# Kernel optimization log

Hardware: AMD Instinct MI355X
Metric: run time of the kernel (lower is better)

Reference implementation:

```python
import jax, jax.numpy as jnp
import numpy as np

ALPHA = 0.9
EPS = 0.01
LAMBDA_PENALTY = 1.0
THRESHOLD = 0.8
COS_EPS = 1e-8
N, F, E = 8192, 256, 262144


def setup_inputs() -> dict:
    key = jax.random.key(0)
    k1, k2, k3, k4, k5 = jax.random.split(key, 5)
    z = jax.random.normal(k1, (N, F), dtype=jnp.float32)
    x_hat = jax.random.normal(k2, (N, F), dtype=jnp.float32)
    edge_index = jax.random.randint(k3, (2, E), 0, N, dtype=jnp.int64)
    f_k2u = jax.random.randint(k4, (N,), 0, 6, dtype=jnp.int64)
    f_u2k = jax.random.randint(k5, (N,), 0, 32, dtype=jnp.int64)
    return {"z": z, "x_hat": x_hat, "edge_index": edge_index,
            "f_k2u": f_k2u, "f_u2k": f_u2k, "epoch": 10}


def _corrcoef_features(z):
    # torch.corrcoef(z.T): correlation between the F feature columns over N nodes
    zm = z - jnp.mean(z, axis=0, keepdims=True)        # [N, F]
    cov = zm.T @ zm                                    # [F, F] (scale cancels in corr)
    std = jnp.sqrt(jnp.diag(cov))                      # [F]
    cor = cov / (std[:, None] * std[None, :])
    cor = jnp.clip(jnp.nan_to_num(cor), -1.0, 1.0)
    # fill_diagonal_(0)
    return cor * (1.0 - jnp.eye(cor.shape[0], dtype=cor.dtype))


def reference(z, x_hat, edge_index, f_k2u, f_u2k, epoch):
    n, f = z.shape
    zm = z - jnp.mean(z, axis=0, keepdims=True)
    cor = _corrcoef_features(z)                        # [F, F]
    # per-node scalar weight: alpha**f_k2u + (1 - alpha**f_u2k)
    w = (ALPHA ** f_k2u.astype(z.dtype)
         + (1.0 - ALPHA ** f_u2k.astype(z.dtype)))     # [N]
    W = w[:, None] * zm                                # [N, F]
    z2 = z + EPS * (W @ cor)                           # [N, F]

    # homophily (crash=True): per-edge cosine sim, scatter-add by source, degree-normalize
    i, j = edge_index[0], edge_index[1]
    zi, zj = z2[i], z2[j]                              # [E, F] gathers
    num = jnp.sum(zi * zj, axis=1)
    ni = jnp.maximum(jnp.linalg.norm(zi, axis=1), COS_EPS)
    nj = jnp.maximum(jnp.linalg.norm(zj, axis=1), COS_EPS)
    sim = num / (ni * nj)                              # [E]
    scores = jax.ops.segment_sum(sim, i, num_segments=n)
    deg = jax.ops.segment_sum(jnp.ones_like(sim), i, num_segments=n)
    deg = jnp.where(deg == 0, 1.0, deg)
    homophily_loss = -jnp.mean(scores / deg)

    # extra_loss (crash=True): dense NxN similarity masked by dense adjacency
    sim_mat = z2 @ z2.T                                # [N, N]
    adj = jnp.zeros((n, n), dtype=z.dtype)
    adj = adj.at[i, j].set(1.0).at[j, i].set(1.0)
    non_conn = sim_mat * (1.0 - adj)
    penalty = jnp.mean(jnp.where(non_conn > THRESHOLD, non_conn, 0.0))

    return homophily_loss + LAMBDA_PENALTY * penalty
```

## Files before the change

kernel.cpp:

```cpp
#include <hip/hip_runtime.h>
#include <stdint.h>
#include <math.h>

#define EPS_C 0.01f
#define THRESH 0.8f

constexpr int Nn = 8192;
constexpr int Ff = 256;
constexpr int Ee = 262144;

__device__ __forceinline__ float b2f(unsigned short u) {
  union { uint32_t i; float f; } v; v.i = ((uint32_t)u) << 16; return v.f;
}
__device__ __forceinline__ unsigned short f2b(float f) {
  union { uint32_t i; float f; } v; v.f = f;
  uint32_t r = v.i + 0x7FFFu + ((v.i >> 16) & 1u);
  return (unsigned short)(r >> 16);
}

typedef __bf16 bf16x8 __attribute__((ext_vector_type(8)));
typedef float f32x4 __attribute__((ext_vector_type(4)));

__global__ void k_transpose(const float* __restrict__ z, unsigned short* __restrict__ zT,
                            float* __restrict__ colsum) {
  __shared__ float Ls[64][65];
  int n0 = blockIdx.x * 64;
  int c0 = blockIdx.y * 64;
  int t = threadIdx.x;
  int r = t >> 4;
  int cq = t & 15;
#pragma unroll
  for (int i = 0; i < 4; ++i) {
    int row = r + 16 * i;
    float4 v = *(const float4*)(z + (size_t)(n0 + row) * Ff + c0 + cq * 4);
    Ls[row][cq * 4 + 0] = v.x;
    Ls[row][cq * 4 + 1] = v.y;
    Ls[row][cq * 4 + 2] = v.z;
    Ls[row][cq * 4 + 3] = v.w;
  }
  __syncthreads();
  if (t < 64) {
    float s = 0.f;
#pragma unroll
    for (int rr = 0; rr < 64; ++rr) s += Ls[rr][t];
    atomicAdd(&colsum[c0 + t], s);
  }
  int cr = t >> 4;
  int nq = t & 15;
#pragma unroll
  for (int i = 0; i < 4; ++i) {
    int c = cr + 16 * i;
    ushort4 o;
    o.x = f2b(Ls[nq * 4 + 0][c]);
    o.y = f2b(Ls[nq * 4 + 1][c]);
    o.z = f2b(Ls[nq * 4 + 2][c]);
    o.w = f2b(Ls[nq * 4 + 3][c]);
    *(ushort4*)(zT + (size_t)(c0 + c) * Nn + n0 + nq * 4) = o;
  }
}

__global__ __launch_bounds__(256, 2) void k_covg(const unsigned short* __restrict__ zT,
                                                 float* __restrict__ covp) {
  int bx = blockIdx.x, by = blockIdx.y, p = blockIdx.z;
  __shared__ __align__(16) unsigned short As[128 * 64];
  __shared__ __align__(16) unsigned short Bs[128 * 64];
  int t = threadIdx.x;
  int lane = t & 63, wv = t >> 6;
  int wr = wv >> 1, wc = wv & 1;
  int quad = lane >> 4, l15 = lane & 15;
  int a0 = by * 128, b0 = bx * 128;

  f32x4 acc[4][4];
#pragma unroll
  for (int i = 0; i < 4; ++i)
#pragma unroll
    for (int j = 0; j < 4; ++j) acc[i][j] = (f32x4){0.f, 0.f, 0.f, 0.f};

  for (int kk = 0; kk < 8; ++kk) {
    int k0 = p * 512 + kk * 64;
#pragma unroll
    for (int it = 0; it < 4; ++it) {
      int s = it * 256 + t;
      int r = s >> 3;
      int g = (s & 7) ^ (r & 7);
      const unsigned short* ga = zT + (size_t)(a0 + r) * Nn + k0 + g * 8;
      const unsigned short* gb = zT + (size_t)(b0 + r) * Nn + k0 + g * 8;
      __builtin_amdgcn_global_load_lds((const __attribute__((address_space(1))) void*)ga,
                                       (__attribute__((address_space(3))) void*)(As + s * 8),
                                       16, 0, 0);
      __builtin_amdgcn_global_load_lds((const __attribute__((address_space(1))) void*)gb,
                                       (__attribute__((address_space(3))) void*)(Bs + s * 8),
                                       16, 0, 0);
    }
    __syncthreads();
#pragma unroll
    for (int kc = 0; kc < 2; ++kc) {
      bf16x8 afr[4], bfr[4];
#pragma unroll
      for (int mt = 0; mt < 4; ++mt) {
        int rA = wr * 64 + mt * 16 + l15;
        int g = kc * 4 + quad;
        int gl = g ^ (rA & 7);
        afr[mt] = *(const bf16x8*)(As + ((size_t)rA * 8 + gl) * 8);
      }
#pragma unroll
      for (int nt = 0; nt < 4; ++nt) {
        int rB = wc * 64 + nt * 16 + l15;
        int g = kc * 4 + quad;
        int gl = g ^ (rB & 7);
        bfr[nt] = *(const bf16x8*)(Bs + ((size_t)rB * 8 + gl) * 8);
      }
#pragma unroll
      for (int mt = 0; mt < 4; ++mt)
#pragma unroll
        for (int nt = 0; nt < 4; ++nt)
          acc[mt][nt] = __builtin_amdgcn_mfma_f32_16x16x32_bf16(afr[mt], bfr[nt],
                                                                acc[mt][nt], 0, 0, 0);
    }
    __syncthreads();
  }

  float* outp = covp + (size_t)p * 65536;
#pragma unroll
  for (int mt = 0; mt < 4; ++mt)
#pragma unroll
    for (int r = 0; r < 4; ++r) {
      int a = a0 + wr * 64 + mt * 16 + quad * 4 + r;
#pragma unroll
      for (int nt = 0; nt < 4; ++nt) {
        int b = b0 + wc * 64 + nt * 16 + l15;
        outp[(size_t)a * Ff + b] = acc[mt][nt][r];
      }
    }
}

__global__ void k_cor(const float* __restrict__ covp, const float* __restrict__ colsum,
                      float* __restrict__ cor) {
  __shared__ float sd[256];
  int a = blockIdx.x, b = threadIdx.x;
  float mb = colsum[b] * (1.f / 8192.f);
  float gb = 0.f;
#pragma unroll
  for (int p = 0; p < 16; ++p) gb += covp[(size_t)p * 65536 + b * 257];
  float sb = sqrtf(gb - 8192.f * mb * mb);
  sd[b] = sb;
  float g = 0.f;
#pragma unroll
  for (int p = 0; p < 16; ++p) g += covp[(size_t)p * 65536 + a * Ff + b];
  __syncthreads();
  float c = 0.f;
  if (a != b) {
    float ma = colsum[a] * (1.f / 8192.f);
    float cv = g - 8192.f * ma * mb;
    c = cv / (sd[a] * sb);
    if (c != c) c = 0.f;
    c = fminf(1.f, fmaxf(-1.f, c));
  }
  cor[a * Ff + b] = c;
}

__global__ __launch_bounds__(256) void k_z2(const float* __restrict__ z,
    const float* __restrict__ colsum, const int* __restrict__ k2u,
    const int* __restrict__ u2k, const float* __restrict__ cor,
    unsigned short* __restrict__ z2b, unsigned char* __restrict__ z2f8,
    float* __restrict__ norms) {
  __shared__ float Wl[16 * 256];
  __shared__ float ws_[16];
  int t = threadIdx.x;
  int row0 = blockIdx.x * 16;
  if (t < 16) {
    int row = row0 + t;
    ws_[t] = powf(0.9f, (float)k2u[row]) + 1.f - powf(0.9f, (float)u2k[row]);
  }
  __syncthreads();
  float mt = colsum[t] * (1.f / 8192.f);
#pragma unroll
  for (int rr = 0; rr < 16; ++rr) {
    int row = row0 + rr;
    Wl[rr * 256 + t] = ws_[rr] * (z[(size_t)row * Ff + t] - mt);
  }
  __syncthreads();
  int tc = t & 63, tr = t >> 6;
  float acc[4][4];
#pragma unroll
  for (int i = 0; i < 4; ++i)
#pragma unroll
    for (int j = 0; j < 4; ++j) acc[i][j] = 0.f;
  const float* corc = cor + tc * 4;
  for (int k = 0; k < 256; ++k) {
    float4 c4 = *(const float4*)(corc + (size_t)k * 256);
#pragma unroll
    for (int rr = 0; rr < 4; ++rr) {
      float wv = Wl[(tr * 4 + rr) * 256 + k];
      acc[rr][0] = fmaf(wv, c4.x, acc[rr][0]);
      acc[rr][1] = fmaf(wv, c4.y, acc[rr][1]);
      acc[rr][2] = fmaf(wv, c4.z, acc[rr][2]);
      acc[rr][3] = fmaf(wv, c4.w, acc[rr][3]);
    }
  }
#pragma unroll
  for (int rr = 0; rr < 4; ++rr) {
    int row = row0 + tr * 4 + rr;
    float4 zv = *(const float4*)(z + (size_t)row * Ff + tc * 4);
    float x0 = zv.x + EPS_C * acc[rr][0];
    float x1 = zv.y + EPS_C * acc[rr][1];
    float x2 = zv.z + EPS_C * acc[rr][2];
    float x3 = zv.w + EPS_C * acc[rr][3];
    ushort4 o;
    o.x = f2b(x0); o.y = f2b(x1); o.z = f2b(x2); o.w = f2b(x3);
    *(ushort4*)(z2b + (size_t)row * Ff + tc * 4) = o;
    int pk = __builtin_amdgcn_cvt_pk_fp8_f32(x0, x1, 0, 0);
    pk = __builtin_amdgcn_cvt_pk_fp8_f32(x2, x3, pk, 1);
    *(unsigned int*)(z2f8 + (size_t)row * Ff + tc * 4) = (unsigned int)pk;
    float s = x0 * x0 + x1 * x1 + x2 * x2 + x3 * x3;
#pragma unroll
    for (int m = 1; m < 64; m <<= 1) s += __shfl_xor(s, m);
    if (tc == 0) norms[row] = fmaxf(sqrtf(s), 1e-8f);
  }
}

__global__ void k_adj(const int* __restrict__ ei, const int* __restrict__ ej,
                      unsigned int* __restrict__ adj) {
  int e = blockIdx.x * 256 + threadIdx.x;
  unsigned int i = (unsigned int)ei[e], j = (unsigned int)ej[e];
  size_t b1 = (size_t)i * Nn + j;
  size_t b2 = (size_t)j * Nn + i;
  atomicOr(&adj[b1 >> 5], 1u << (b1 & 31));
  atomicOr(&adj[b2 >> 5], 1u << (b2 & 31));
}

__global__ __launch_bounds__(256) void k_edge(const int* __restrict__ ei,
                       const int* __restrict__ ej,
                       const unsigned short* __restrict__ z2b,
                       const float* __restrict__ norms,
                       float* __restrict__ scores, float* __restrict__ deg) {
  int t = threadIdx.x;
  int wv = t >> 6, lane = t & 63;
  int half = lane >> 5;
  int l32 = lane & 31;
  int gw = blockIdx.x * 4 + wv;
  int ebase = gw * 32;
#pragma unroll 2
  for (int it = 0; it < 16; ++it) {
    int e = ebase + it * 2 + half;
    int i = ei[e], j = ej[e];
    uint4 ua = *(const uint4*)(z2b + (size_t)i * Ff + l32 * 8);
    uint4 ub = *(const uint4*)(z2b + (size_t)j * Ff + l32 * 8);
    float d = 0.f;
    const uint32_t* pa = (const uint32_t*)&ua;
    const uint32_t* pb = (const uint32_t*)&ub;
#pragma unroll
    for (int q = 0; q < 4; ++q) {
      union { uint32_t u; float f; } alo, ahi, blo, bhi;
      alo.u = pa[q] << 16;  ahi.u = pa[q] & 0xffff0000u;
      blo.u = pb[q] << 16;  bhi.u = pb[q] & 0xffff0000u;
      d = fmaf(alo.f, blo.f, d);
      d = fmaf(ahi.f, bhi.f, d);
    }
#pragma unroll
    for (int m = 1; m < 32; m <<= 1) d += __shfl_xor(d, m);
    if (l32 == 0) {
      float sim = d / (norms[i] * norms[j]);
      atomicAdd(&scores[i], sim);
      atomicAdd(&deg[i], 1.f);
    }
  }
}

__global__ __launch_bounds__(256, 4) void k_penalty(const unsigned char* __restrict__ z2f8,
    const unsigned int* __restrict__ adj, float* __restrict__ pp) {
  int tb = blockIdx.x;
  int br = (int)(64.5 - sqrt(64.5 * 64.5 - 2.0 * (double)tb));
  while ((br + 1) * 64 - ((br + 1) * br) / 2 <= tb) ++br;
  while (br * 64 - (br * (br - 1)) / 2 > tb) --br;
  int bc = br + (tb - (br * 64 - (br * (br - 1)) / 2));

  __shared__ __align__(16) unsigned char LB[32768];
  int t = threadIdx.x;
  int lane = t & 63;
  int wv = t >> 6;
  int wr = wv >> 1, wc = wv & 1;
  int quad = lane >> 4;
  int l15 = lane & 15;
  int arow0 = br * 128, brow0 = bc * 128;

  f32x4 acc[4][4];
#pragma unroll
  for (int i = 0; i < 4; ++i)
#pragma unroll
    for (int j = 0; j < 4; ++j) acc[i][j] = (f32x4){0.f, 0.f, 0.f, 0.f};

#define ISSUE_PHASE(p)                                                                   \
  {                                                                                      \
    unsigned char* buf = LB + ((p) & 1) * 16384;                                         \
    int k0 = (p) * 64;                                                                   \
    _Pragma("unroll")                                                                    \
    for (int it = 0; it < 2; ++it) {                                                     \
      int s = it * 256 + t;                                                              \
      int r = s >> 2;                                                                    \
      int gs = (s & 3) ^ (r & 3) ^ ((r >> 2) & 3);                                       \
      const unsigned char* ga = z2f8 + (size_t)(arow0 + r) * Ff + k0 + gs * 16;          \
      const unsigned char* gb = z2f8 + (size_t)(brow0 + r) * Ff + k0 + gs * 16;          \
      __builtin_amdgcn_global_load_lds((const __attribute__((address_space(1))) void*)ga,\
                                       (__attribute__((address_space(3))) void*)(buf + s * 16),      \
                                       16, 0, 0);                                        \
      __builtin_amdgcn_global_load_lds((const __attribute__((address_space(1))) void*)gb,\
                                       (__attribute__((address_space(3))) void*)(buf + 8192 + s * 16),\
                                       16, 0, 0);                                        \
    }                                                                                    \
  }

  ISSUE_PHASE(0)
  ISSUE_PHASE(1)
#pragma unroll
  for (int p = 0; p < 4; ++p) {
    if (p < 3) __builtin_amdgcn_s_waitcnt(0xF74);
    else       __builtin_amdgcn_s_waitcnt(0xF70);
    __builtin_amdgcn_s_barrier();
    const unsigned char* As = LB + (p & 1) * 16384;
    const unsigned char* Bs = As + 8192;
#pragma unroll
    for (int kc = 0; kc < 2; ++kc) {
      long a8[4], b8[4];
      int gidx = kc * 2 + (quad >> 1);
      int bo = (quad & 1) * 8;
#pragma unroll
      for (int mt = 0; mt < 4; ++mt) {
        int rA = wr * 64 + mt * 16 + l15;
        int gl = gidx ^ (rA & 3) ^ ((rA >> 2) & 3);
        a8[mt] = *(const long*)(As + rA * 64 + gl * 16 + bo);
      }
#pragma unroll
      for (int nt = 0; nt < 4; ++nt) {
        int rB = wc * 64 + nt * 16 + l15;
        int gl = gidx ^ (rB & 3) ^ ((rB >> 2) & 3);
        b8[nt] = *(const long*)(Bs + rB * 64 + gl * 16 + bo);
      }
#pragma unroll
      for (int mt = 0; mt < 4; ++mt)
#pragma unroll
        for (int nt = 0; nt < 4; ++nt)
          acc[mt][nt] = __builtin_amdgcn_mfma_f32_16x16x32_fp8_fp8(a8[mt], b8[nt],
                                                                   acc[mt][nt], 0, 0, 0);
    }
    __builtin_amdgcn_s_barrier();
    if (p < 2) ISSUE_PHASE(p + 2)
  }
#undef ISSUE_PHASE

  float local = 0.f;
  int a_base = arow0 + wr * 64;
  int b_base = brow0 + wc * 64;
#pragma unroll
  for (int mt = 0; mt < 4; ++mt) {
#pragma unroll
    for (int r = 0; r < 4; ++r) {
      int a = a_base + mt * 16 + quad * 4 + r;
      uint64_t bits = *(const uint64_t*)(adj + (size_t)a * 256 + (b_base >> 5));
#pragma unroll
      for (int nt = 0; nt < 4; ++nt) {
        float v = acc[mt][nt][r];
        int boff = nt * 16 + l15;
        bool conn = (bits >> boff) & 1ull;
        float wgt;
        if (br != bc) wgt = 2.f;
        else {
          int b = b_base + boff;
          wgt = (a < b) ? 2.f : (a == b ? 1.f : 0.f);
        }
        if (!conn && v > THRESH) local += wgt * v;
      }
    }
  }
#pragma unroll
  for (int m = 1; m < 64; m <<= 1) local += __shfl_xor(local, m);
  float* red = (float*)LB;
  if (lane == 0) red[wv] = local;
  __syncthreads();
  if (t == 0) pp[tb] = red[0] + red[1] + red[2] + red[3];
}

__global__ void k_final(const float* __restrict__ scores, const float* __restrict__ deg,
                        const float* __restrict__ pp, float* __restrict__ out) {
  __shared__ float redh[4];
  __shared__ float redp[4];
  int t = threadIdx.x;
  float acch = 0.f;
#pragma unroll 4
  for (int it = 0; it < 32; ++it) {
    int n = it * 256 + t;
    float dg = deg[n];
    acch += scores[n] / (dg == 0.f ? 1.f : dg);
  }
  float accp = 0.f;
#pragma unroll
  for (int it = 0; it < 9; ++it) {
    int idx = it * 256 + t;
    if (idx < 2080) accp += pp[idx];
  }
#pragma unroll
  for (int m = 1; m < 64; m <<= 1) {
    acch += __shfl_xor(acch, m);
    accp += __shfl_xor(accp, m);
  }
  if ((t & 63) == 0) { redh[t >> 6] = acch; redp[t >> 6] = accp; }
  __syncthreads();
  if (t == 0) {
    double h = -(double)(redh[0] + redh[1] + redh[2] + redh[3]) / 8192.0;
    double p = (double)(redp[0] + redp[1] + redp[2] + redp[3]) / (8192.0 * 8192.0);
    out[0] = (float)(h + p);
  }
}

extern "C" void kernel_launch(void* const* d_in, const int* in_sizes, int n_in,
                              void* d_out, int out_size, void* d_ws, size_t ws_size,
                              hipStream_t stream) {
  const float* z = (const float*)d_in[0];
  const int* ei = (const int*)d_in[2];
  const int* ej = ei + Ee;
  const int* k2u = (const int*)d_in[3];
  const int* u2k = (const int*)d_in[4];

  char* ws = (char*)d_ws;
  unsigned int* adj = (unsigned int*)(ws);
  float* colsum     = (float*)(ws + 8388608);
  float* scores     = (float*)(ws + 8389632);
  float* deg        = (float*)(ws + 8422400);
  const size_t ZERO_BYTES = 8455168;
  float* covp       = (float*)(ws + 8455296);
  unsigned short* zT  = (unsigned short*)(ws + 12649600);
  unsigned short* z2b = (unsigned short*)(ws + 16843904);
  float* cor        = (float*)(ws + 21038208);
  float* norms      = (float*)(ws + 21300352);
  float* pp         = (float*)(ws + 21333120);
  unsigned char* z2f8 = (unsigned char*)(ws + 21341568);

  hipMemsetAsync(d_ws, 0, ZERO_BYTES, stream);
  k_adj<<<1024, 256, 0, stream>>>(ei, ej, adj);
  k_transpose<<<dim3(128, 4), 256, 0, stream>>>(z, zT, colsum);
  k_covg<<<dim3(2, 2, 16), 256, 0, stream>>>(zT, covp);
  k_cor<<<256, 256, 0, stream>>>(covp, colsum, cor);
  k_z2<<<512, 256, 0, stream>>>(z, colsum, k2u, u2k, cor, z2b, z2f8, norms);
  k_edge<<<2048, 256, 0, stream>>>(ei, ej, z2b, norms, scores, deg);
  k_penalty<<<2080, 256, 0, stream>>>(z2f8, adj, pp);
  k_final<<<1, 256, 0, stream>>>(scores, deg, pp, (float*)d_out);
}
```

Baseline: 209.1 us.

## Use MI355 scaled fp8 16x16x128 MFMA with whole-K LDS staging in penalty GEMM

Switches the penalty kernel from the 16x16x32 fp8 MFMA to the gfx950 scaled f8f6f4 16x16x128 instruction with unit scales, so each wave issues a quarter as many MFMAs. The K dimension is now staged in two 128-wide phases held in a 64KB LDS buffer, both issued up front, with a new 8-way XOR swizzle and 16-byte LDS reads. Launch bounds drop to 2 blocks per SM to fit the larger shared memory, which lowers occupancy. A barrier is added before reusing LDS for the final reduction.

```diff
diff --git a/kernel.cpp b/kernel.cpp
--- a/kernel.cpp
+++ b/kernel.cpp
@@ -20,6 +20,8 @@
 
 typedef __bf16 bf16x8 __attribute__((ext_vector_type(8)));
 typedef float f32x4 __attribute__((ext_vector_type(4)));
+typedef int i32x4 __attribute__((ext_vector_type(4)));
+typedef int i32x8 __attribute__((ext_vector_type(8)));
 
 __global__ void k_transpose(const float* __restrict__ z, unsigned short* __restrict__ zT,
                             float* __restrict__ colsum) {
@@ -267,7 +269,7 @@
   }
 }
 
-__global__ __launch_bounds__(256, 4) void k_penalty(const unsigned char* __restrict__ z2f8,
+__global__ __launch_bounds__(256, 2) void k_penalty(const unsigned char* __restrict__ z2f8,
     const unsigned int* __restrict__ adj, float* __restrict__ pp) {
   int tb = blockIdx.x;
   int br = (int)(64.5 - sqrt(64.5 * 64.5 - 2.0 * (double)tb));
@@ -275,7 +277,7 @@
   while (br * 64 - (br * (br - 1)) / 2 > tb) --br;
   int bc = br + (tb - (br * 64 - (br * (br - 1)) / 2));
 
-  __shared__ __align__(16) unsigned char LB[32768];
+  __shared__ __align__(16) unsigned char LB[65536];
   int t = threadIdx.x;
   int lane = t & 63;
   int wv = t >> 6;
@@ -292,20 +294,20 @@
 
 #define ISSUE_PHASE(p)                                                                   \
   {                                                                                      \
-    unsigned char* buf = LB + ((p) & 1) * 16384;                                         \
-    int k0 = (p) * 64;                                                                   \
+    unsigned char* buf = LB + (p) * 32768;                                               \
+    int k0 = (p) * 128;                                                                  \
     _Pragma("unroll")                                                                    \
-    for (int it = 0; it < 2; ++it) {                                                     \
+    for (int it = 0; it < 4; ++it) {                                                     \
       int s = it * 256 + t;                                                              \
-      int r = s >> 2;                                                                    \
-      int gs = (s & 3) ^ (r & 3) ^ ((r >> 2) & 3);                                       \
-      const unsigned char* ga = z2f8 + (size_t)(arow0 + r) * Ff + k0 + gs * 16;          \
-      const unsigned char* gb = z2f8 + (size_t)(brow0 + r) * Ff + k0 + gs * 16;          \
+      int r = s >> 3;                                                                    \
+      int g = (s & 7) ^ (r & 7);                                                         \
+      const unsigned char* ga = z2f8 + (size_t)(arow0 + r) * Ff + k0 + g * 16;           \
+      const unsigned char* gb = z2f8 + (size_t)(brow0 + r) * Ff + k0 + g * 16;           \
       __builtin_amdgcn_global_load_lds((const __attribute__((address_space(1))) void*)ga,\
                                        (__attribute__((address_space(3))) void*)(buf + s * 16),      \
                                        16, 0, 0);                                        \
       __builtin_amdgcn_global_load_lds((const __attribute__((address_space(1))) void*)gb,\
-                                       (__attribute__((address_space(3))) void*)(buf + 8192 + s * 16),\
+                                       (__attribute__((address_space(3))) void*)(buf + 16384 + s * 16),\
                                        16, 0, 0);                                        \
     }                                                                                    \
   }
@@ -313,38 +315,36 @@
   ISSUE_PHASE(0)
   ISSUE_PHASE(1)
 #pragma unroll
-  for (int p = 0; p < 4; ++p) {
-    if (p < 3) __builtin_amdgcn_s_waitcnt(0xF74);
-    else       __builtin_amdgcn_s_waitcnt(0xF70);
+  for (int p = 0; p < 2; ++p) {
+    if (p == 0) __builtin_amdgcn_s_waitcnt(0xF78);
+    else        __builtin_amdgcn_s_waitcnt(0xF70);
     __builtin_amdgcn_s_barrier();
-    const unsigned char* As = LB + (p & 1) * 16384;
-    const unsigned char* Bs = As + 8192;
-#pragma unroll
-    for (int kc = 0; kc < 2; ++kc) {
-      long a8[4], b8[4];
-      int gidx = kc * 2 + (quad >> 1);
-      int bo = (quad & 1) * 8;
-#pragma unroll
-      for (int mt = 0; mt < 4; ++mt) {
-        int rA = wr * 64 + mt * 16 + l15;
-        int gl = gidx ^ (rA & 3) ^ ((rA >> 2) & 3);
-        a8[mt] = *(const long*)(As + rA * 64 + gl * 16 + bo);
-      }
-#pragma unroll
-      for (int nt = 0; nt < 4; ++nt) {
-        int rB = wc * 64 + nt * 16 + l15;
-        int gl = gidx ^ (rB & 3) ^ ((rB >> 2) & 3);
-        b8[nt] = *(const long*)(Bs + rB * 64 + gl * 16 + bo);
-      }
-#pragma unroll
-      for (int mt = 0; mt < 4; ++mt)
-#pragma unroll
-        for (int nt = 0; nt < 4; ++nt)
-          acc[mt][nt] = __builtin_amdgcn_mfma_f32_16x16x32_fp8_fp8(a8[mt], b8[nt],
-                                                                   acc[mt][nt], 0, 0, 0);
-    }
-    __builtin_amdgcn_s_barrier();
-    if (p < 2) ISSUE_PHASE(p + 2)
+    const unsigned char* As = LB + p * 32768;
+    const unsigned char* Bs = As + 16384;
+    i32x8 a8[4], b8[4];
+#pragma unroll
+    for (int mt = 0; mt < 4; ++mt) {
+      int rA = wr * 64 + mt * 16 + l15;
+      int g0 = (2 * quad) ^ (rA & 7), g1 = (2 * quad + 1) ^ (rA & 7);
+      i32x4 lo = *(const i32x4*)(As + rA * 128 + g0 * 16);
+      i32x4 hi = *(const i32x4*)(As + rA * 128 + g1 * 16);
+      a8[mt] = (i32x8){lo[0], lo[1], lo[2], lo[3], hi[0], hi[1], hi[2], hi[3]};
+    }
+#pragma unroll
+    for (int nt = 0; nt < 4; ++nt) {
+      int rB = wc * 64 + nt * 16 + l15;
+      int g0 = (2 * quad) ^ (rB & 7), g1 = (2 * quad + 1) ^ (rB & 7);
+      i32x4 lo = *(const i32x4*)(Bs + rB * 128 + g0 * 16);
+      i32x4 hi = *(const i32x4*)(Bs + rB * 128 + g1 * 16);
+      b8[nt] = (i32x8){lo[0], lo[1], lo[2], lo[3], hi[0], hi[1], hi[2], hi[3]};
+    }
+#pragma unroll
+    for (int mt = 0; mt < 4; ++mt)
+#pragma unroll
+      for (int nt = 0; nt < 4; ++nt)
+        acc[mt][nt] = __builtin_amdgcn_mfma_scale_f32_16x16x128_f8f6f4(
+            a8[mt], b8[nt], acc[mt][nt], 0, 0,
+            0, 0x7F7F7F7F, 0, 0x7F7F7F7F);
   }
 #undef ISSUE_PHASE
 
@@ -374,6 +374,7 @@
   }
 #pragma unroll
   for (int m = 1; m < 64; m <<= 1) local += __shfl_xor(local, m);
+  __syncthreads();
   float* red = (float*)LB;
   if (lane == 0) red[wv] = local;
   __syncthreads();
```

Result: no change. 205.1 us (-2.0%).
